# Kernel tuning notes

Measured on AMD Instinct MI355X. Metric: run time of the kernel, lower is better.

## Reference

```python
import jax, jax.numpy as jnp
import numpy as np

ALPHA = 0.5
DECAY = 0.5
THR = 0.5

B, T, N_IN, N_HID = 64, 256, 128, 2048


def setup_inputs() -> dict:
    key = jax.random.key(0)
    k1, k2, k3, k4, k5 = jax.random.split(key, 5)
    x = jax.random.normal(k1, (B, T, N_IN), dtype=jnp.float32)
    W_in = jax.random.uniform(k2, (N_IN, N_HID), minval=-0.1, maxval=0.1, dtype=jnp.float32)
    A = jax.random.uniform(k3, (N_HID, N_HID), minval=-0.1, maxval=0.1, dtype=jnp.float32)
    bias = jax.random.uniform(k4, (N_HID,), minval=-1.0, maxval=1.0, dtype=jnp.float32)
    mem0 = jax.random.uniform(k5, (B, N_HID), minval=0.0, maxval=0.2, dtype=jnp.float32)
    return {"x": x, "W_in": W_in, "A": A, "bias": bias, "mem0": mem0}


def reference(x, W_in, A, bias, mem0):
    # x: [B, T, N_in] -> outputs mems, spikes: [1, B, T, N_hid]
    spike0 = jnp.zeros_like(mem0)

    def step(carry, x_t):
        mem, spike = carry
        U = x_t @ W_in                      # [B, N_hid]
        r = spike @ A                       # [B, N_hid]
        y = jnp.tanh(ALPHA * r + (1.0 - ALPHA) * (U + bias))
        mem = mem * DECAY - THR * (1.0 - spike) + y
        spike = (mem > THR).astype(jnp.float32)
        return (mem, spike), (mem, spike)

    xs = jnp.swapaxes(x, 0, 1)              # [T, B, N_in]
    _, (mems_t, spikes_t) = jax.lax.scan(step, (mem0, spike0), xs)
    mems = jnp.swapaxes(mems_t, 0, 1)[None]     # [1, B, T, N_hid]
    spikes = jnp.swapaxes(spikes_t, 0, 1)[None]  # [1, B, T, N_hid]
    return mems, spikes
```

## Files before the change

kernel.cpp:

```cpp
#include <hip/hip_runtime.h>
#include <math.h>

#define B_   64
#define T_   256
#define NIN  128
#define NH   2048
#define NTHR 512

typedef unsigned int  u32;
typedef unsigned short u16;
typedef unsigned long long u64;
typedef __attribute__((ext_vector_type(8))) short bf16x8;
typedef __attribute__((ext_vector_type(4))) float f32x4;
typedef __attribute__((ext_vector_type(4))) u32   u32x4;

#define OFF_AHI  0
#define OFF_ALO  65792
#define OFF_CRED 131584
#define SMEM_BYTES 148992


__device__ __forceinline__ u16 f2bf(float f) {
    u32 u = __float_as_uint(f);
    return (u16)((u + 0x7FFFu + ((u >> 16) & 1u)) >> 16);
}
__device__ __forceinline__ float bf2f(u16 h) { return __uint_as_float(((u32)h) << 16); }

__device__ __forceinline__ float zthrf_of(float c) {
    if (c >= 1.f)  return  __builtin_inff();
    if (c <= -1.f) return -__builtin_inff();
    return 0.5f * logf((1.f + c) / (1.f - c));
}

__global__ __launch_bounds__(256, 2) void u_init(
    const float* __restrict__ x, const float* __restrict__ W_in,
    const float* __restrict__ bias, float* __restrict__ u_out)
{
    __shared__ float xS[32 * 132];
    const int tid = threadIdx.x, bid = blockIdx.x;
    const int row0 = bid * 32;
    for (int idx = tid; idx < 32 * NIN; idx += 256) {
        int r = idx >> 7, k = idx & 127;
        xS[r * 132 + k] = x[(size_t)(row0 + r) * NIN + k];
    }
    __syncthreads();

    float bc[4][2];
#pragma unroll
    for (int cg = 0; cg < 2; ++cg)
#pragma unroll
        for (int q = 0; q < 4; ++q)
            bc[q][cg] = bias[cg * 1024 + q * 256 + tid];

    for (int cg = 0; cg < 2; ++cg) {
        for (int rg = 0; rg < 2; ++rg) {
            float acc[4][16];
#pragma unroll
            for (int q = 0; q < 4; ++q)
#pragma unroll
                for (int r = 0; r < 16; ++r) acc[q][r] = 0.f;
            for (int kc = 0; kc < 8; ++kc) {
                float w[4][16];
#pragma unroll
                for (int q = 0; q < 4; ++q)
#pragma unroll
                    for (int kk = 0; kk < 16; ++kk)
                        w[q][kk] = W_in[(size_t)(kc * 16 + kk) * NH + cg * 1024 + q * 256 + tid];
#pragma unroll
                for (int r = 0; r < 16; ++r) {
                    const f32x4* xv = (const f32x4*)(xS + (rg * 16 + r) * 132 + kc * 16);
#pragma unroll
                    for (int v = 0; v < 4; ++v) {
                        f32x4 xx = xv[v];
#pragma unroll
                        for (int q = 0; q < 4; ++q) {
                            acc[q][r] = fmaf(xx.x, w[q][v * 4 + 0], acc[q][r]);
                            acc[q][r] = fmaf(xx.y, w[q][v * 4 + 1], acc[q][r]);
                            acc[q][r] = fmaf(xx.z, w[q][v * 4 + 2], acc[q][r]);
                            acc[q][r] = fmaf(xx.w, w[q][v * 4 + 3], acc[q][r]);
                        }
                    }
                }
            }
#pragma unroll
            for (int r = 0; r < 16; ++r)
#pragma unroll
                for (int q = 0; q < 4; ++q)
                    u_out[(size_t)(row0 + rg * 16 + r) * NH + cg * 1024 + q * 256 + tid]
                        = 0.5f * (acc[q][r] + bc[q][cg]);
        }
    }
}

__global__ __launch_bounds__(NTHR, 2) void persist(
    const float* __restrict__ A,
    const float* __restrict__ mem0,
    float* __restrict__ out_mem,
    float* out_spk,
    u32* __restrict__ spkbuf)
{
    extern __shared__ char smem[];
    u16*   AhiS = (u16*)(smem + OFF_AHI);
    u16*   AloS = (u16*)(smem + OFF_ALO);
    float* cred = (float*)(smem + OFF_CRED);

    const int tid = threadIdx.x;
    const int bid = blockIdx.x;
    const int cb  = bid & 127;
    const int bg  = bid >> 7;
    const int c0  = cb * 16;

    for (int idx = tid; idx < NH * 16; idx += NTHR) {
        int i = idx >> 4, c = idx & 15;
        float a = A[(size_t)i * NH + c0 + c];
        u16 hi = f2bf(a);
        AhiS[c * 2056 + i] = hi;
        AloS[c * 2056 + i] = f2bf(a - bf2f(hi));
    }

    const int n   = tid & 15;
    const int bl  = tid >> 4;
    const int b   = bg * 32 + bl;
    const int col = c0 + n;
    double m = (double)mem0[(size_t)b * NH + col];
    double sprev = 0.0;
    float zthrf = zthrf_of((float)(1.0 - 0.5 * m));

    const int lane = tid & 63, wave = tid >> 6;
    const int qn = lane & 15, quad = lane >> 4;
    const int mt = wave & 1;
    const int kp = wave >> 1;
    const u32 sh = ((u32)(quad & 1) * 8) + ((u32)(quad >> 1) * 16);

    float up = out_spk[(size_t)b * T_ * NH + col];

    u32* stgW = (u32*)smem + wave * 320;

    const u32* pollbase = spkbuf
        + (size_t)(bg * 32 + mt * 16 + (lane >> 2)) * 128 + kp * 32 + (lane & 3) * 8;

    __syncthreads();

    bf16x8 Ah[16], Al[16];
#pragma unroll
    for (int ktl = 0; ktl < 16; ++ktl) {
        int kt = kp * 16 + ktl;
        Ah[ktl] = *(const bf16x8*)(AhiS + qn * 2056 + quad * 8 + kt * 32);
        Al[ktl] = *(const bf16x8*)(AloS + qn * 2056 + quad * 8 + kt * 32);
    }
#pragma unroll
    for (int i = 0; i < 16; ++i)
        asm volatile("" : "+v"(Ah[i]), "+v"(Al[i]));

    __syncthreads();

    for (int t = 0; t < T_; ++t) {
        const u32* src = pollbase + ((t & 1) ? 8192 : 0);
        const u32 te = (u32)t << 16;
        u32x4 da, db;
        int guard = 0;
        while (true) {
            asm volatile(
                "global_load_dwordx4 %0, %2, off sc1\n\t"
                "global_load_dwordx4 %1, %2, off offset:16 sc1\n\t"
                "s_waitcnt vmcnt(0)"
                : "=&v"(da), "=&v"(db)
                : "v"(src)
                : "memory");
            u32 bad = (da.x ^ te) | (da.y ^ te) | (da.z ^ te) | (da.w ^ te)
                    | (db.x ^ te) | (db.y ^ te) | (db.z ^ te) | (db.w ^ te);
            if (!(bad >> 16)) break;
            if (++guard > 30000) break;
            if (guard > 1) __builtin_amdgcn_s_sleep(1);
        }

        float upn = 0.f;
        if (t + 1 < T_) upn = out_spk[((size_t)b * T_ + t + 1) * NH + col];

        u32x4 pk;
        pk.x = (da.x & 0xFFFFu) | (da.y << 16);
        pk.y = (da.z & 0xFFFFu) | (da.w << 16);
        pk.z = (db.x & 0xFFFFu) | (db.y << 16);
        pk.w = (db.z & 0xFFFFu) | (db.w << 16);
        *(u32x4*)(stgW + (lane >> 2) * 20 + (lane & 3) * 4) = pk;
        asm volatile("s_waitcnt lgkmcnt(0)" ::: "memory");

        u32 sw[16];
        {
            const u32x4* rp = (const u32x4*)(stgW + qn * 20);
            u32x4 s0 = rp[0], s1 = rp[1], s2 = rp[2], s3 = rp[3];
            sw[0] = s0.x; sw[1] = s0.y; sw[2]  = s0.z; sw[3]  = s0.w;
            sw[4] = s1.x; sw[5] = s1.y; sw[6]  = s1.z; sw[7]  = s1.w;
            sw[8] = s2.x; sw[9] = s2.y; sw[10] = s2.z; sw[11] = s2.w;
            sw[12] = s3.x; sw[13] = s3.y; sw[14] = s3.z; sw[15] = s3.w;
        }

        f32x4 ac0 = {0.f,0.f,0.f,0.f}, ac1 = {0.f,0.f,0.f,0.f};
        f32x4 ac2 = {0.f,0.f,0.f,0.f}, ac3 = {0.f,0.f,0.f,0.f};
#pragma unroll
        for (int ktl = 0; ktl < 4; ++ktl) {
#pragma unroll
            for (int c = 0; c < 4; ++c) {
                int k = c * 4 + ktl;
                u32 byte = (sw[k] >> sh) & 255u;
                u32x4 aw;
                aw.x = ((byte & 1u)   ? 0x3F80u : 0u) | ((byte & 2u)   ? 0x3F800000u : 0u);
                aw.y = ((byte & 4u)   ? 0x3F80u : 0u) | ((byte & 8u)   ? 0x3F800000u : 0u);
                aw.z = ((byte & 16u)  ? 0x3F80u : 0u) | ((byte & 32u)  ? 0x3F800000u : 0u);
                aw.w = ((byte & 64u)  ? 0x3F80u : 0u) | ((byte & 128u) ? 0x3F800000u : 0u);
                bf16x8 af = __builtin_bit_cast(bf16x8, aw);
                f32x4* ac = (c == 0) ? &ac0 : (c == 1) ? &ac1 : (c == 2) ? &ac2 : &ac3;
                *ac = __builtin_amdgcn_mfma_f32_16x16x32_bf16(af, Ah[k], *ac, 0, 0, 0);
                *ac = __builtin_amdgcn_mfma_f32_16x16x32_bf16(af, Al[k], *ac, 0, 0, 0);
            }
        }
        f32x4 acc = (ac0 + ac1) + (ac2 + ac3);
        float* cw = cred + (t & 1) * 2176;
#pragma unroll
        for (int reg = 0; reg < 4; ++reg)
            cw[((kp * 2 + mt) * 16 + quad * 4 + reg) * 17 + qn] = acc[reg];
        __syncthreads();

        float r = 0.f;
#pragma unroll
        for (int p = 0; p < 4; ++p)
            r += cw[((p * 2 + (bl >> 4)) * 16 + (bl & 15)) * 17 + n];

        float zf = 0.5f * r + up;
        int sp = zf > zthrf;

        u64 bal = __ballot(sp);
        if (n == 0) {
            u32 bits = (u32)((bal >> ((bl & 3) * 16)) & 0xFFFFull);
            u32 val = ((u32)(t + 1) << 16) | bits;
            u32* dst = spkbuf + ((t & 1) ? 0 : 8192) + b * 128 + cb;
            __hip_atomic_store(dst, val, __ATOMIC_RELAXED, __HIP_MEMORY_SCOPE_AGENT);
        }

        float y = tanhf(zf);
        m = m * 0.5 - 0.5 * (1.0 - sprev) + (double)y;
        size_t o = ((size_t)b * T_ + t) * NH + col;
        out_mem[o] = (float)m;
        out_spk[o] = sp ? 1.f : 0.f;
        sprev = sp ? 1.0 : 0.0;
        zthrf = zthrf_of((float)(1.0 - 0.5 * m - 0.5 * sprev));
        up = upn;
    }
}

extern "C" void kernel_launch(void* const* d_in, const int* in_sizes, int n_in,
                              void* d_out, int out_size, void* d_ws, size_t ws_size,
                              hipStream_t stream) {
    const float* x    = (const float*)d_in[0];
    const float* W_in = (const float*)d_in[1];
    const float* A    = (const float*)d_in[2];
    const float* bias = (const float*)d_in[3];
    const float* mem0 = (const float*)d_in[4];

    float* out_mem = (float*)d_out;
    float* out_spk = out_mem + (size_t)B_ * T_ * NH;
    u32*   spkbuf  = (u32*)d_ws;

    (void)hipFuncSetAttribute((const void*)persist,
                              hipFuncAttributeMaxDynamicSharedMemorySize, SMEM_BYTES);

    hipMemsetAsync(spkbuf, 0, 2 * 64 * 128 * sizeof(u32), stream);
    hipLaunchKernelGGL(u_init, dim3(512), dim3(256), 0, stream, x, W_in, bias, out_spk);
    hipLaunchKernelGGL(persist, dim3(256), dim3(NTHR), SMEM_BYTES, stream,
                       A, mem0, out_mem, out_spk, spkbuf);
}
```

Measured before the change: 1.124 ms.

## Compute input projection with bf16 split-precision MFMA tiles

Rewrites the x·W_in + bias precompute kernel to stage 128x128 tiles of x and W_in in LDS as hi/lo bf16 pairs. Each tile is then computed with four 16x16x32 bf16 MFMAs per block, replacing scalar fp32 FMAs. The aim is to cut the time of the pre-recurrence GEMM by using the matrix cores. The split-bf16 scheme keeps near-fp32 accuracy at four times the MFMA work. The grid grows to 2048 blocks, and each block uses about 136 KB of dynamic LDS.

```diff
diff --git a/kernel.cpp b/kernel.cpp
--- a/kernel.cpp
+++ b/kernel.cpp
@@ -19,6 +19,8 @@
 #define OFF_CRED 131584
 #define SMEM_BYTES 148992
 
+#define USMEM (4 * 128 * 136 * 2)
+
 
 __device__ __forceinline__ u16 f2bf(float f) {
     u32 u = __float_as_uint(f);
@@ -32,63 +34,85 @@
     return 0.5f * logf((1.f + c) / (1.f - c));
 }
 
-__global__ __launch_bounds__(256, 2) void u_init(
+__global__ __launch_bounds__(512) void u_init(
     const float* __restrict__ x, const float* __restrict__ W_in,
     const float* __restrict__ bias, float* __restrict__ u_out)
 {
-    __shared__ float xS[32 * 132];
+    extern __shared__ char us[];
+    u16* WhS = (u16*)us;
+    u16* WlS = WhS + 128 * 136;
+    u16* XhS = WlS + 128 * 136;
+    u16* XlS = XhS + 128 * 136;
+
     const int tid = threadIdx.x, bid = blockIdx.x;
-    const int row0 = bid * 32;
-    for (int idx = tid; idx < 32 * NIN; idx += 256) {
-        int r = idx >> 7, k = idx & 127;
-        xS[r * 132 + k] = x[(size_t)(row0 + r) * NIN + k];
+    const int gr = bid >> 4;
+    const int gc = bid & 15;
+
+    for (int i = tid; i < 128 * 128; i += 512) {
+        int c = i & 127, k = i >> 7;
+        float w = 0.5f * W_in[(size_t)k * NH + gc * 128 + c];
+        u16 wh = f2bf(w);
+        WhS[c * 136 + k] = wh;
+        WlS[c * 136 + k] = f2bf(w - bf2f(wh));
+        float xv = x[(size_t)(gr * 128 + k) * NIN + c];
+        u16 xh = f2bf(xv);
+        XhS[k * 136 + c] = xh;
+        XlS[k * 136 + c] = f2bf(xv - bf2f(xh));
     }
     __syncthreads();
 
-    float bc[4][2];
-#pragma unroll
-    for (int cg = 0; cg < 2; ++cg)
-#pragma unroll
-        for (int q = 0; q < 4; ++q)
-            bc[q][cg] = bias[cg * 1024 + q * 256 + tid];
-
-    for (int cg = 0; cg < 2; ++cg) {
-        for (int rg = 0; rg < 2; ++rg) {
-            float acc[4][16];
-#pragma unroll
-            for (int q = 0; q < 4; ++q)
-#pragma unroll
-                for (int r = 0; r < 16; ++r) acc[q][r] = 0.f;
-            for (int kc = 0; kc < 8; ++kc) {
-                float w[4][16];
-#pragma unroll
-                for (int q = 0; q < 4; ++q)
-#pragma unroll
-                    for (int kk = 0; kk < 16; ++kk)
-                        w[q][kk] = W_in[(size_t)(kc * 16 + kk) * NH + cg * 1024 + q * 256 + tid];
-#pragma unroll
-                for (int r = 0; r < 16; ++r) {
-                    const f32x4* xv = (const f32x4*)(xS + (rg * 16 + r) * 132 + kc * 16);
-#pragma unroll
-                    for (int v = 0; v < 4; ++v) {
-                        f32x4 xx = xv[v];
-#pragma unroll
-                        for (int q = 0; q < 4; ++q) {
-                            acc[q][r] = fmaf(xx.x, w[q][v * 4 + 0], acc[q][r]);
-                            acc[q][r] = fmaf(xx.y, w[q][v * 4 + 1], acc[q][r]);
-                            acc[q][r] = fmaf(xx.z, w[q][v * 4 + 2], acc[q][r]);
-                            acc[q][r] = fmaf(xx.w, w[q][v * 4 + 3], acc[q][r]);
-                        }
-                    }
-                }
+    const int lane = tid & 63, wave = tid >> 6;
+    const int qn = lane & 15, quad = lane >> 4;
+    const int mt = wave & 1;
+    const int nc = wave >> 1;
+
+    bf16x8 Wh[2][4], Wl[2][4];
+#pragma unroll
+    for (int ct = 0; ct < 2; ++ct)
+#pragma unroll
+        for (int kt = 0; kt < 4; ++kt) {
+            int c = (nc * 2 + ct) * 16 + qn;
+            Wh[ct][kt] = *(const bf16x8*)(WhS + c * 136 + kt * 32 + quad * 8);
+            Wl[ct][kt] = *(const bf16x8*)(WlS + c * 136 + kt * 32 + quad * 8);
+        }
+
+    f32x4 acc[4][2];
+#pragma unroll
+    for (int rt = 0; rt < 4; ++rt)
+#pragma unroll
+        for (int ct = 0; ct < 2; ++ct) acc[rt][ct] = (f32x4){0.f, 0.f, 0.f, 0.f};
+
+#pragma unroll
+    for (int rt = 0; rt < 4; ++rt) {
+        int r = mt * 64 + rt * 16 + qn;
+        bf16x8 Xh[4], Xl[4];
+#pragma unroll
+        for (int kt = 0; kt < 4; ++kt) {
+            Xh[kt] = *(const bf16x8*)(XhS + r * 136 + kt * 32 + quad * 8);
+            Xl[kt] = *(const bf16x8*)(XlS + r * 136 + kt * 32 + quad * 8);
+        }
+#pragma unroll
+        for (int ct = 0; ct < 2; ++ct)
+#pragma unroll
+            for (int kt = 0; kt < 4; ++kt) {
+                acc[rt][ct] = __builtin_amdgcn_mfma_f32_16x16x32_bf16(Xh[kt], Wh[ct][kt], acc[rt][ct], 0, 0, 0);
+                acc[rt][ct] = __builtin_amdgcn_mfma_f32_16x16x32_bf16(Xh[kt], Wl[ct][kt], acc[rt][ct], 0, 0, 0);
+                acc[rt][ct] = __builtin_amdgcn_mfma_f32_16x16x32_bf16(Xl[kt], Wh[ct][kt], acc[rt][ct], 0, 0, 0);
+                acc[rt][ct] = __builtin_amdgcn_mfma_f32_16x16x32_bf16(Xl[kt], Wl[ct][kt], acc[rt][ct], 0, 0, 0);
             }
-#pragma unroll
-            for (int r = 0; r < 16; ++r)
-#pragma unroll
-                for (int q = 0; q < 4; ++q)
-                    u_out[(size_t)(row0 + rg * 16 + r) * NH + cg * 1024 + q * 256 + tid]
-                        = 0.5f * (acc[q][r] + bc[q][cg]);
-        }
+    }
+
+#pragma unroll
+    for (int ct = 0; ct < 2; ++ct) {
+        int col = gc * 128 + (nc * 2 + ct) * 16 + qn;
+        float bc = 0.5f * bias[col];
+#pragma unroll
+        for (int rt = 0; rt < 4; ++rt)
+#pragma unroll
+            for (int reg = 0; reg < 4; ++reg) {
+                int row = gr * 128 + mt * 64 + rt * 16 + quad * 4 + reg;
+                u_out[(size_t)row * NH + col] = acc[rt][ct][reg] + bc;
+            }
     }
 }
 
@@ -263,9 +287,12 @@
 
     (void)hipFuncSetAttribute((const void*)persist,
                               hipFuncAttributeMaxDynamicSharedMemorySize, SMEM_BYTES);
+    (void)hipFuncSetAttribute((const void*)u_init,
+                              hipFuncAttributeMaxDynamicSharedMemorySize, USMEM);
 
     hipMemsetAsync(spkbuf, 0, 2 * 64 * 128 * sizeof(u32), stream);
-    hipLaunchKernelGGL(u_init, dim3(512), dim3(256), 0, stream, x, W_in, bias, out_spk);
+    hipLaunchKernelGGL(u_init, dim3(2048), dim3(512), USMEM, stream,
+                       x, W_in, bias, out_spk);
     hipLaunchKernelGGL(persist, dim3(256), dim3(NTHR), SMEM_BYTES, stream,
                        A, mem0, out_mem, out_spk, spkbuf);
 }
```

After: 1.168 ms. 1.04x slower.
